# Kernel optimization log

Measured on AMD Instinct MI355X. Metric: run time of the kernel, lower is better.

## Reference

```python
import jax, jax.numpy as jnp
import numpy as np

B, S, H = 2, 2048, 3072
NH, NKV, HD = 24, 8, 128  # num_heads, num_kv_heads, head_dim


def setup_inputs() -> dict:
    key = jax.random.key(0)
    ks = jax.random.split(key, 5)
    scale = 0.02
    return {
        "hidden_states": jax.random.normal(ks[0], (B, S, H), dtype=jnp.float32),
        "attention_mask": jnp.zeros((B, 1, S, S), dtype=jnp.float32),
        "Wq": jax.random.normal(ks[1], (H, NH * HD), dtype=jnp.float32) * scale,
        "Wk": jax.random.normal(ks[2], (H, NKV * HD), dtype=jnp.float32) * scale,
        "Wv": jax.random.normal(ks[3], (H, NKV * HD), dtype=jnp.float32) * scale,
        "Wo": jax.random.normal(ks[4], (NH * HD, H), dtype=jnp.float32) * scale,
    }


def reference(hidden_states, attention_mask, Wq, Wk, Wv, Wo):
    b, s, _ = hidden_states.shape
    n_rep = NH // NKV
    # projections
    q = (hidden_states @ Wq).reshape(b, s, NH, HD).transpose(0, 2, 1, 3)   # [B,NH,S,D]
    k = (hidden_states @ Wk).reshape(b, s, NKV, HD).transpose(0, 2, 1, 3)  # [B,NKV,S,D]
    v = (hidden_states @ Wv).reshape(b, s, NKV, HD).transpose(0, 2, 1, 3)
    # grouped-query attention: view q as [B, NKV, n_rep, S, D]; avoids materializing repeated KV
    qg = q.reshape(b, NKV, n_rep, s, HD)
    scores = jnp.einsum("bgrqd,bgkd->bgrqk", qg, k) / jnp.sqrt(jnp.float32(HD))
    scores = scores.reshape(b, NH, s, s) + attention_mask
    attn = jax.nn.softmax(scores.astype(jnp.float32), axis=-1).astype(q.dtype)
    out = jnp.einsum("bgrqk,bgkd->bgrqd", attn.reshape(b, NKV, n_rep, s, s), v)
    out = out.reshape(b, NH, s, HD).transpose(0, 2, 1, 3).reshape(b, s, NH * HD)
    return out @ Wo
```

## Files before the change

kernel.cpp:

```cpp
#include <hip/hip_runtime.h>
#include <hip/hip_bf16.h>
#include <stdint.h>

typedef __attribute__((ext_vector_type(8))) short short8;
typedef __attribute__((ext_vector_type(4))) float f32x4;
typedef __attribute__((ext_vector_type(16))) float f32x16;

#define DEVINL static __device__ __forceinline__

DEVINL unsigned short f2bf(float x) {
  union { float f; unsigned int u; } c; c.f = x;
  unsigned int u = c.u;
  u += 0x7fffu + ((u >> 16) & 1u);
  return (unsigned short)(u >> 16);
}

DEVINL f32x4 mfma16(short8 a, short8 b, f32x4 c) {
  return __builtin_amdgcn_mfma_f32_16x16x32_bf16(a, b, c, 0, 0, 0);
}

DEVINL f32x16 mfma32(short8 a, short8 b, f32x16 c) {
  return __builtin_amdgcn_mfma_f32_32x32x16_bf16(a, b, c, 0, 0, 0);
}

DEVINL unsigned int cvtpk(float lo, float hi_) {
  unsigned int r;
  asm("v_cvt_pk_bf16_f32 %0, %1, %2" : "=v"(r) : "v"(lo), "v"(hi_));
  return r;
}

DEVINL void pl32swap(unsigned int& a, unsigned int& b) {
  asm("v_permlane32_swap_b32 %0, %1" : "+v"(a), "+v"(b));
}

DEVINL void gload16(const void* g, void* l) {
  __builtin_amdgcn_global_load_lds((const __attribute__((address_space(1))) void*)g,
                                   (__attribute__((address_space(3))) void*)l, 16, 0, 0);
}

static constexpr int BB = 2, SS = 2048, HH = 3072;
static constexpr int NH = 24, NKV = 8, HD = 128, NREP = 3;
static constexpr int MM = BB * SS;
static constexpr int KQ = NH * HD;
static constexpr int KKV = NKV * HD;
static constexpr int KV2 = 2 * KKV;

__global__ void k_cvt(const float* __restrict__ in, unsigned short* __restrict__ out,
                      int n, float scale) {
  int i = (blockIdx.x * 256 + threadIdx.x) * 4;
  if (i >= n) return;
  float4 v = *reinterpret_cast<const float4*>(in + i);
  ushort4 o;
  o.x = f2bf(v.x * scale); o.y = f2bf(v.y * scale);
  o.z = f2bf(v.z * scale); o.w = f2bf(v.w * scale);
  *reinterpret_cast<ushort4*>(out + i) = o;
}

__global__ void k_zero(int* p) { *p = 0; }

__global__ void k_flag(const float* __restrict__ in, int n4, int* __restrict__ flag) {
  int i = blockIdx.x * 256 + threadIdx.x;
  if (i >= n4) return;
  float4 v = reinterpret_cast<const float4*>(in)[i];
  bool nz = (v.x != 0.f) || (v.y != 0.f) || (v.z != 0.f) || (v.w != 0.f);
  if (__any(nz) && (threadIdx.x & 63) == 0) atomicOr(flag, 1);
}

__global__ void k_tcvt(const float* __restrict__ in, unsigned short* __restrict__ out,
                       int R, int C, float scale) {
  __shared__ float t[32][33];
  int tx = threadIdx.x & 31, ty = threadIdx.x >> 5;
  int r0 = blockIdx.y * 32, c0 = blockIdx.x * 32;
#pragma unroll
  for (int i = 0; i < 32; i += 8)
    t[ty + i][tx] = in[(long)(r0 + ty + i) * C + c0 + tx];
  __syncthreads();
#pragma unroll
  for (int i = 0; i < 32; i += 8)
    out[(long)(c0 + ty + i) * R + r0 + tx] = f2bf(t[tx][ty + i] * scale);
}

__global__ void k_vt(const unsigned short* __restrict__ KV, unsigned short* __restrict__ VT) {
  __shared__ unsigned short t[32][33];
  int b = blockIdx.z >> 3, kv = blockIdx.z & 7;
  int tx = threadIdx.x & 31, ty = threadIdx.x >> 5;
  int d0 = blockIdx.x * 32, s0 = blockIdx.y * 32;
  const unsigned short* src = KV + ((long)b * SS) * KV2 + KKV + kv * HD;
  unsigned short* dst = VT + (long)(b * NKV + kv) * HD * SS;
#pragma unroll
  for (int i = 0; i < 32; i += 8)
    t[ty + i][tx] = src[(long)(s0 + ty + i) * KV2 + d0 + tx];
  __syncthreads();
#pragma unroll
  for (int i = 0; i < 32; i += 8)
    dst[(long)(d0 + ty + i) * SS + s0 + tx] = t[tx][ty + i];
}

template <typename OutT>
__global__ __launch_bounds__(256, 3) void k_gemm(const unsigned short* __restrict__ A,
                                                 const unsigned short* __restrict__ Bt,
                                                 OutT* __restrict__ C,
                                                 int M, int N, int K) {
  __shared__ alignas(16) unsigned short As[128 * 64];
  __shared__ alignas(16) unsigned short Bs[128 * 64];
  const int tid = threadIdx.x;
  const int wave = tid >> 6, lane = tid & 63;
  const int l15 = lane & 15, g = lane >> 4;
  const int wr = wave >> 1, wc = wave & 1;
  const long m0 = (long)blockIdx.y * 128, n0 = (long)blockIdx.x * 128;

  f32x4 acc[4][4] = {{{0.f,0.f,0.f,0.f}}};

  for (long k0 = 0; k0 < K; k0 += 64) {
#pragma unroll
    for (int j = 0; j < 4; ++j) {
      int idx = j * 256 + wave * 64 + lane;
      int row = idx >> 3, sub = idx & 7;
      int sc_ = (sub ^ (row & 7)) * 8;
      gload16(A  + (m0 + row) * K + k0 + sc_, (char*)As + (j * 4 + wave) * 1024);
      gload16(Bt + (n0 + row) * K + k0 + sc_, (char*)Bs + (j * 4 + wave) * 1024);
    }
    __syncthreads();
#pragma unroll
    for (int ks = 0; ks < 2; ++ks) {
      short8 a[4], b[4];
#pragma unroll
      for (int m = 0; m < 4; ++m) {
        int row = wr * 64 + m * 16 + l15;
        int cb = (ks * 64 + g * 16) ^ ((row & 7) << 4);
        a[m] = *reinterpret_cast<const short8*>((const char*)As + row * 128 + cb);
      }
#pragma unroll
      for (int n = 0; n < 4; ++n) {
        int row = wc * 64 + n * 16 + l15;
        int cb = (ks * 64 + g * 16) ^ ((row & 7) << 4);
        b[n] = *reinterpret_cast<const short8*>((const char*)Bs + row * 128 + cb);
      }
#pragma unroll
      for (int m = 0; m < 4; ++m)
#pragma unroll
        for (int n = 0; n < 4; ++n)
          acc[m][n] = mfma16(a[m], b[n], acc[m][n]);
    }
    __syncthreads();
  }

#pragma unroll
  for (int m = 0; m < 4; ++m)
#pragma unroll
    for (int n = 0; n < 4; ++n)
#pragma unroll
      for (int r = 0; r < 4; ++r) {
        long row = m0 + wr * 64 + m * 16 + g * 4 + r;
        long col = n0 + wc * 64 + n * 16 + l15;
        float v = acc[m][n][r];
        if constexpr (sizeof(OutT) == 2) C[row * N + col] = f2bf(v);
        else                             C[row * N + col] = v;
      }
}

__global__ __launch_bounds__(256, 3) void k_attn(const unsigned short* __restrict__ Q,
                                                 const unsigned short* __restrict__ KV,
                                                 const unsigned short* __restrict__ VT,
                                                 const float* __restrict__ Mb,
                                                 unsigned short* __restrict__ AO,
                                                 const int* __restrict__ flagp) {
  const int tid = threadIdx.x;
  const int wave = tid >> 6, lane = tid & 63;
  const int l31 = lane & 31, hi = lane >> 5;

  const int bid = blockIdx.x;
  const int id = (bid & 7) * 96 + (bid >> 3);
  const int qt = id & 15;
  const int h  = (id >> 4) % NH;
  const int b  = id / (16 * NH);
  const int kv = h / NREP;
  const int qb = qt * 128 + wave * 32;

  const unsigned short* Qp = Q + ((long)b * SS + qb) * KQ + h * HD;
  const unsigned short* Kp = KV + (long)b * SS * KV2 + kv * HD;
  const unsigned short* Vp = VT + (long)(b * NKV + kv) * HD * SS;
  const float* Mp = Mb + ((long)b * SS + qb + l31) * SS + hi * 4;

  const int msknz = *flagp;
  const float LOG2E = 1.4426950408889634f;

  __shared__ alignas(16) unsigned short Ks[2][64 * 128];
  __shared__ alignas(16) unsigned short Vs[128 * 64];

  int koff[8], voff[4];
#pragma unroll
  for (int c = 0; c < 8; ++c) {
    int s = c * 2 + hi;
    koff[c] = l31 * 256 + (((s & 8) | ((s ^ (l31 & 7)) & 7)) << 4);
  }
#pragma unroll
  for (int ks = 0; ks < 4; ++ks)
    voff[ks] = l31 * 128 + (((ks * 2 + hi) ^ (l31 & 7)) << 4);

  short8 qf[8];
#pragma unroll
  for (int c = 0; c < 8; ++c)
    qf[c] = *reinterpret_cast<const short8*>(Qp + (long)l31 * KQ + c * 16 + hi * 8);

  f32x16 o[4];
#pragma unroll
  for (int dc = 0; dc < 4; ++dc)
#pragma unroll
    for (int r = 0; r < 16; ++r) o[dc][r] = 0.f;
  float mrun = -3e38f, lrun = 0.f;

  auto stageK = [&](int buf, int kt) {
#pragma unroll
    for (int j = 0; j < 4; ++j) {
      int idx = j * 256 + wave * 64 + lane;
      int row = idx >> 4, s = idx & 15;
      int ss = (s & 8) | ((s ^ row) & 7);
      gload16(Kp + (long)(kt + row) * KV2 + ss * 8,
              (char*)Ks[buf] + (j * 4 + wave) * 1024);
    }
  };
  auto stageV = [&](int kt) {
#pragma unroll
    for (int j = 0; j < 4; ++j) {
      int idx = j * 256 + wave * 64 + lane;
      int row = idx >> 3, s = idx & 7;
      int ss = s ^ (row & 7);
      gload16(Vp + (long)row * SS + kt + ss * 8,
              (char*)Vs + (j * 4 + wave) * 1024);
    }
  };

  stageK(0, 0);
  __syncthreads();

  for (int t = 0; t < SS / 64; ++t) {
    const int kt = t * 64;
    const bool last = (t == SS / 64 - 1);
    stageV(kt);
    if (!last) stageK((t + 1) & 1, kt + 64);

    float4 mk[8];
    if (msknz) {
#pragma unroll
      for (int sb = 0; sb < 2; ++sb)
#pragma unroll
        for (int u = 0; u < 4; ++u)
          mk[sb * 4 + u] = *reinterpret_cast<const float4*>(Mp + kt + sb * 32 + u * 8);
    }

    f32x16 sc0, sc1;
#pragma unroll
    for (int r = 0; r < 16; ++r) { sc0[r] = 0.f; sc1[r] = 0.f; }
    __builtin_amdgcn_s_setprio(1);
#pragma unroll
    for (int sb = 0; sb < 2; ++sb) {
      const char* kbp = (const char*)Ks[t & 1] + sb * 8192;
#pragma unroll
      for (int c = 0; c < 8; ++c) {
        short8 kf = *reinterpret_cast<const short8*>(kbp + koff[c]);
        if (sb == 0) sc0 = mfma32(kf, qf[c], sc0);
        else         sc1 = mfma32(kf, qf[c], sc1);
      }
    }
    __builtin_amdgcn_s_setprio(0);

    if (msknz) {
#pragma unroll
      for (int sb = 0; sb < 2; ++sb)
#pragma unroll
        for (int u = 0; u < 4; ++u)
#pragma unroll
          for (int e = 0; e < 4; ++e) {
            int r = u * 4 + e;
            if (sb) sc1[r] = fmaf((&mk[sb * 4 + u].x)[e], LOG2E, sc1[r]);
            else    sc0[r] = fmaf((&mk[sb * 4 + u].x)[e], LOG2E, sc0[r]);
          }
    }
    float ta = -3e38f, tb = -3e38f, tc = -3e38f, td = -3e38f;
#pragma unroll
    for (int r = 0; r < 8; ++r) {
      ta = fmaxf(ta, sc0[r]); tb = fmaxf(tb, sc0[r + 8]);
      tc = fmaxf(tc, sc1[r]); td = fmaxf(td, sc1[r + 8]);
    }
    float tm = fmaxf(fmaxf(ta, tb), fmaxf(tc, td));
    tm = fmaxf(tm, __shfl_xor(tm, 32));

    if (!__all(tm <= mrun + 8.f)) {
      float mn = fmaxf(mrun, tm);
      float corr = __builtin_amdgcn_exp2f(mrun - mn);
      mrun = mn;
      lrun *= corr;
#pragma unroll
      for (int r = 0; r < 16; ++r) {
        int qrow = (r & 3) + 8 * (r >> 2) + 4 * hi;
        float cr = __shfl(corr, qrow);
#pragma unroll
        for (int dc = 0; dc < 4; ++dc) o[dc][r] *= cr;
      }
    }

    float s0a = 0.f, s0b = 0.f, s1a = 0.f, s1b = 0.f;
#pragma unroll
    for (int r = 0; r < 8; ++r) {
      sc0[r]     = __builtin_amdgcn_exp2f(sc0[r] - mrun);     s0a += sc0[r];
      sc0[r + 8] = __builtin_amdgcn_exp2f(sc0[r + 8] - mrun); s0b += sc0[r + 8];
      sc1[r]     = __builtin_amdgcn_exp2f(sc1[r] - mrun);     s1a += sc1[r];
      sc1[r + 8] = __builtin_amdgcn_exp2f(sc1[r + 8] - mrun); s1b += sc1[r + 8];
    }
    float ts = (s0a + s0b) + (s1a + s1b);
    ts += __shfl_xor(ts, 32);
    lrun += ts;

    if (!last) asm volatile("s_waitcnt vmcnt(4)" ::: "memory");
    else       asm volatile("s_waitcnt vmcnt(0)" ::: "memory");
    __builtin_amdgcn_s_barrier();

    __builtin_amdgcn_s_setprio(1);
#pragma unroll
    for (int ks = 0; ks < 4; ++ks) {
      const int R = 8 * (ks & 1);
      unsigned int A0, A1, B0, B1;
      if (ks < 2) {
        A0 = cvtpk(sc0[R + 0], sc0[R + 1]); A1 = cvtpk(sc0[R + 2], sc0[R + 3]);
        B0 = cvtpk(sc0[R + 4], sc0[R + 5]); B1 = cvtpk(sc0[R + 6], sc0[R + 7]);
      } else {
        A0 = cvtpk(sc1[R + 0], sc1[R + 1]); A1 = cvtpk(sc1[R + 2], sc1[R + 3]);
        B0 = cvtpk(sc1[R + 4], sc1[R + 5]); B1 = cvtpk(sc1[R + 6], sc1[R + 7]);
      }
      pl32swap(A0, B0);
      pl32swap(A1, B1);
      union { unsigned int w[4]; short8 v; } pa;
      pa.w[0] = A0; pa.w[1] = A1; pa.w[2] = B0; pa.w[3] = B1;
#pragma unroll
      for (int dc = 0; dc < 4; ++dc) {
        short8 vf = *reinterpret_cast<const short8*>((const char*)Vs + dc * 4096 + voff[ks]);
        o[dc] = mfma32(pa.v, vf, o[dc]);
      }
    }
    __builtin_amdgcn_s_setprio(0);

    __syncthreads();
  }

  float inv = 1.f / lrun;
#pragma unroll
  for (int r = 0; r < 16; ++r) {
    int qrow = (r & 3) + 8 * (r >> 2) + 4 * hi;
    float ir = __shfl(inv, qrow);
    long row = qb + qrow;
#pragma unroll
    for (int dc = 0; dc < 4; ++dc)
      AO[((long)b * SS + row) * KQ + h * HD + dc * 32 + l31] = f2bf(o[dc][r] * ir);
  }
}

extern "C" void kernel_launch(void* const* d_in, const int* in_sizes, int n_in,
                              void* d_out, int out_size, void* d_ws, size_t ws_size,
                              hipStream_t stream) {
  const float* hidden = (const float*)d_in[0];
  const float* mask   = (const float*)d_in[1];
  const float* Wq     = (const float*)d_in[2];
  const float* Wk     = (const float*)d_in[3];
  const float* Wv     = (const float*)d_in[4];
  const float* Wo     = (const float*)d_in[5];

  char* ws = (char*)d_ws;
  constexpr long SZ_X   = (long)MM * HH * 2;
  constexpr long SZ_WQT = (long)HH * KQ * 2;
  constexpr long SZ_WKT = (long)HH * KKV * 2;
  constexpr long SZ_QKV = (long)MM * KKV * 2;
  unsigned short* Xb  = (unsigned short*)(ws);
  unsigned short* WqT = (unsigned short*)(ws + SZ_X);
  unsigned short* WkT = (unsigned short*)(ws + SZ_X + SZ_WQT);
  unsigned short* WvT = (unsigned short*)(ws + SZ_X + SZ_WQT + SZ_WKT);
  unsigned short* WoT = (unsigned short*)(ws + SZ_X + SZ_WQT + 2 * SZ_WKT);
  unsigned short* Qb  = (unsigned short*)(ws + SZ_X + 2 * SZ_WQT + 2 * SZ_WKT);
  unsigned short* KVb = (unsigned short*)(ws + 2 * SZ_X + 2 * SZ_WQT + 2 * SZ_WKT);
  unsigned short* VTb = (unsigned short*)(ws + 2 * SZ_X + 2 * SZ_WQT + 2 * SZ_WKT + 2 * SZ_QKV);
  unsigned short* AOb = (unsigned short*)(ws + 2 * SZ_X + 2 * SZ_WQT + 2 * SZ_WKT + 3 * SZ_QKV);
  int* flagp = (int*)Xb;

  const float QSCALE = 0.08838834764831845f * 1.4426950408889634f;

  k_cvt<<<(MM * HH) / 1024, 256, 0, stream>>>(hidden, Xb, MM * HH, 1.0f);
  k_tcvt<<<dim3(KQ / 32, HH / 32), 256, 0, stream>>>(Wq, WqT, HH, KQ, QSCALE);
  k_tcvt<<<dim3(KKV / 32, HH / 32), 256, 0, stream>>>(Wk, WkT, HH, KKV, 1.0f);
  k_tcvt<<<dim3(KKV / 32, HH / 32), 256, 0, stream>>>(Wv, WvT, HH, KKV, 1.0f);
  k_tcvt<<<dim3(KQ / 32, HH / 32), 256, 0, stream>>>(Wo, WoT, KQ, HH, 1.0f);

  k_gemm<unsigned short><<<dim3(KQ / 128, MM / 128), 256, 0, stream>>>(Xb, WqT, Qb, MM, KQ, HH);
  k_gemm<unsigned short><<<dim3(KV2 / 128, MM / 128), 256, 0, stream>>>(Xb, WkT, KVb, MM, KV2, HH);

  k_vt<<<dim3(HD / 32, SS / 32, BB * NKV), 256, 0, stream>>>(KVb, VTb);
  k_zero<<<1, 1, 0, stream>>>(flagp);
  k_flag<<<(BB * SS * SS / 4 + 255) / 256, 256, 0, stream>>>(mask, BB * SS * SS / 4, flagp);

  k_attn<<<16 * NH * BB, 256, 0, stream>>>(Qb, KVb, VTb, mask, AOb, flagp);

  k_gemm<float><<<dim3(HH / 128, MM / 128), 256, 0, stream>>>(AOb, WoT, (float*)d_out, MM, HH, HH);
}
```

Measured before the change: 458.2 us.

## Add 256x192 double-buffered GEMM kernel for Q and output projections

Introduces a 512-thread GEMM with 256x192 output tiles, swizzled LDS staging, double buffering and wave priority hints. It is used for the Q projection and the output projection in place of the 128x128 kernel. Larger tiles raise operand reuse per load and cut global traffic. The grid shrinks to 16x16 = 256 blocks, about one wave on the device, and register and LDS pressure grow.

```diff
diff --git a/kernel.cpp b/kernel.cpp
--- a/kernel.cpp
+++ b/kernel.cpp
@@ -154,6 +154,108 @@
         long row = m0 + wr * 64 + m * 16 + g * 4 + r;
         long col = n0 + wc * 64 + n * 16 + l15;
         float v = acc[m][n][r];
+        if constexpr (sizeof(OutT) == 2) C[row * N + col] = f2bf(v);
+        else                             C[row * N + col] = v;
+      }
+}
+
+template <typename OutT>
+__global__ __launch_bounds__(512, 2) void k_gemm256(const unsigned short* __restrict__ A,
+                                                    const unsigned short* __restrict__ Bt,
+                                                    OutT* __restrict__ C,
+                                                    int M, int N, int K) {
+  __shared__ alignas(16) unsigned short As[2][256 * 64];
+  __shared__ alignas(16) unsigned short Bs[2][192 * 64];
+  const int tid = threadIdx.x;
+  const int lane = tid & 63;
+  const int l15 = lane & 15, g = lane >> 4;
+  const int wave = tid >> 6;
+  const int wm = wave >> 2, wn = wave & 3;
+
+  const int flat = blockIdx.y * gridDim.x + blockIdx.x;
+  const int swz = (flat & 7) * ((gridDim.x * gridDim.y) >> 3) + (flat >> 3);
+  const long m0 = (long)(swz / gridDim.x) * 256;
+  const long n0 = (long)(swz % gridDim.x) * 192;
+  const int nkt = K >> 6;
+
+  f32x4 acc[8][3];
+#pragma unroll
+  for (int mi = 0; mi < 8; ++mi)
+#pragma unroll
+    for (int ni = 0; ni < 3; ++ni)
+      acc[mi][ni] = f32x4{0.f, 0.f, 0.f, 0.f};
+
+  auto stage = [&](int buf, int kt) {
+#pragma unroll
+    for (int j = 0; j < 4; ++j) {
+      int idx = j * 512 + tid;
+      int row = idx >> 3, s = idx & 7;
+      int ss = s ^ (row & 7);
+      gload16(A + (m0 + row) * K + kt * 64 + ss * 8,
+              (char*)As[buf] + idx * 16);
+    }
+#pragma unroll
+    for (int j = 0; j < 3; ++j) {
+      int idx = j * 512 + tid;
+      int row = idx >> 3, s = idx & 7;
+      int ss = s ^ (row & 7);
+      gload16(Bt + (n0 + row) * K + kt * 64 + ss * 8,
+              (char*)Bs[buf] + idx * 16);
+    }
+  };
+
+  stage(0, 0);
+  __syncthreads();
+
+  for (int kt = 0; kt < nkt; ++kt) {
+    const int cur = kt & 1;
+    if (kt + 1 < nkt) stage(cur ^ 1, kt + 1);
+    const char* Ab = (const char*)As[cur];
+    const char* Bb = (const char*)Bs[cur];
+
+    short8 b[3][2];
+#pragma unroll
+    for (int n = 0; n < 3; ++n) {
+      int R = wn * 48 + n * 16 + l15;
+#pragma unroll
+      for (int kk = 0; kk < 2; ++kk)
+        b[n][kk] = *reinterpret_cast<const short8*>(
+            Bb + R * 128 + (((kk * 4 + g) ^ (R & 7)) << 4));
+    }
+    __builtin_amdgcn_s_setprio(1);
+#pragma unroll
+    for (int mh = 0; mh < 2; ++mh) {
+      short8 a[4][2];
+#pragma unroll
+      for (int m = 0; m < 4; ++m) {
+        int R = wm * 128 + mh * 64 + m * 16 + l15;
+#pragma unroll
+        for (int kk = 0; kk < 2; ++kk)
+          a[m][kk] = *reinterpret_cast<const short8*>(
+              Ab + R * 128 + (((kk * 4 + g) ^ (R & 7)) << 4));
+      }
+#pragma unroll
+      for (int m = 0; m < 4; ++m)
+#pragma unroll
+        for (int n = 0; n < 3; ++n)
+#pragma unroll
+          for (int kk = 0; kk < 2; ++kk)
+            acc[mh * 4 + m][n] = mfma16(a[m][kk], b[n][kk], acc[mh * 4 + m][n]);
+    }
+    __builtin_amdgcn_s_setprio(0);
+
+    __syncthreads();
+  }
+
+#pragma unroll
+  for (int mi = 0; mi < 8; ++mi)
+#pragma unroll
+    for (int ni = 0; ni < 3; ++ni)
+#pragma unroll
+      for (int r = 0; r < 4; ++r) {
+        long row = m0 + wm * 128 + mi * 16 + g * 4 + r;
+        long col = n0 + wn * 48 + ni * 16 + l15;
+        float v = acc[mi][ni][r];
         if constexpr (sizeof(OutT) == 2) C[row * N + col] = f2bf(v);
         else                             C[row * N + col] = v;
       }
@@ -389,7 +491,7 @@
   k_tcvt<<<dim3(KKV / 32, HH / 32), 256, 0, stream>>>(Wv, WvT, HH, KKV, 1.0f);
   k_tcvt<<<dim3(KQ / 32, HH / 32), 256, 0, stream>>>(Wo, WoT, KQ, HH, 1.0f);
 
-  k_gemm<unsigned short><<<dim3(KQ / 128, MM / 128), 256, 0, stream>>>(Xb, WqT, Qb, MM, KQ, HH);
+  k_gemm256<unsigned short><<<dim3(KQ / 192, MM / 256), 512, 0, stream>>>(Xb, WqT, Qb, MM, KQ, HH);
   k_gemm<unsigned short><<<dim3(KV2 / 128, MM / 128), 256, 0, stream>>>(Xb, WkT, KVb, MM, KV2, HH);
 
   k_vt<<<dim3(HD / 32, SS / 32, BB * NKV), 256, 0, stream>>>(KVb, VTb);
@@ -398,5 +500,5 @@
 
   k_attn<<<16 * NH * BB, 256, 0, stream>>>(Qb, KVb, VTb, mask, AOb, flagp);
 
-  k_gemm<float><<<dim3(HH / 128, MM / 128), 256, 0, stream>>>(AOb, WoT, (float*)d_out, MM, HH, HH);
-}
+  k_gemm256<float><<<dim3(HH / 192, MM / 256), 512, 0, stream>>>(AOb, WoT, (float*)d_out, MM, HH, HH);
+}
```

Result: faster. 449.1 us (-2.0%).
